# Optimization experiments

Hardware: AMD Instinct MI355X
Metric: run time of the kernel (lower is better)

The kernel has to match this reference:

```python
import jax, jax.numpy as jnp
import numpy as np

N, D, B = 500000, 128, 2048

def setup_inputs() -> dict:
    key = jax.random.key(0)
    ks = jax.random.split(key, 7)
    x = jax.random.normal(ks[0], (N, D), dtype=jnp.float32)
    batch = jnp.sort(jax.random.randint(ks[1], (N,), 0, B)).astype(jnp.int64)
    s = 1.0 / np.sqrt(D)
    Wm = jax.random.uniform(ks[2], (D, D), jnp.float32, -s, s)  # xavier-ish
    fc1_w = jax.random.uniform(ks[3], (D // 4, D), jnp.float32, -s, s)
    fc1_b = jnp.zeros((D // 4,), jnp.float32)
    fc2_w = jax.random.uniform(ks[4], (D, D // 4), jnp.float32, -1/np.sqrt(D//4), 1/np.sqrt(D//4))
    fc2_b = jnp.zeros((D,), jnp.float32)
    return {"x": x, "batch": batch, "size": B, "Wm": Wm,
            "fc1_w": fc1_w, "fc1_b": fc1_b, "fc2_w": fc2_w, "fc2_b": fc2_b}

def reference(x, batch, size, Wm, fc1_w, fc1_b, fc2_w, fc2_b):
    batch = batch.astype(jnp.int32)
    # fc: Linear -> ReLU -> Linear -> Tanh
    attention = jnp.tanh(jax.nn.relu(x @ fc1_w.T + fc1_b) @ fc2_w.T + fc2_b)
    x2 = attention * x + x  # [N, D]
    # scatter_mean over graphs
    sums = jax.ops.segment_sum(x2, batch, num_segments=size)  # [B, D]
    cnt = jax.ops.segment_sum(jnp.ones((x2.shape[0],), x2.dtype), batch, num_segments=size)
    mean = sums / jnp.maximum(cnt, 1.0)[:, None]
    transformed_global = jnp.tanh(mean @ Wm)  # [B, D]
    coefs = jax.nn.sigmoid(jnp.sum(x2 * transformed_global[batch], axis=1))  # [N]
    weighted = coefs[:, None] * x2
    return jax.ops.segment_sum(weighted, batch, num_segments=size)  # [B, D]
```

## Files before the change

### kernel.cpp

```cpp
#include <hip/hip_runtime.h>
#include <math.h>

#define D 128
#define BLOCKS_A 768
#define BLOCKS_C 1536
#define THREADS 256

typedef short s8v __attribute__((ext_vector_type(8)));
typedef float f4v __attribute__((ext_vector_type(4)));

__device__ __forceinline__ float fast_tanh(float z) {
    float e = __expf(2.f * z);
    return 1.f - 2.f / (e + 1.f);
}
__device__ __forceinline__ unsigned cvt_pk_bf16(float lo, float hi) {
    unsigned r;
    asm("v_cvt_pk_bf16_f32 %0, %1, %2" : "=v"(r) : "v"(lo), "v"(hi));
    return r;
}
__device__ __forceinline__ s8v pack8(float4 w0, float4 w1) {
    union { unsigned u[4]; s8v v; } r;
    r.u[0] = cvt_pk_bf16(w0.x, w0.y);
    r.u[1] = cvt_pk_bf16(w0.z, w0.w);
    r.u[2] = cvt_pk_bf16(w1.x, w1.y);
    r.u[3] = cvt_pk_bf16(w1.z, w1.w);
    return r.v;
}

#define RFLUSH(ACC_, SEG_, DST_)                                              \
    if ((SEG_) >= 0) {                                                        \
        _Pragma("unroll")                                                     \
        for (int t = 0; t < 8; ++t) {                                         \
            ACC_[t] += __shfl_xor(ACC_[t], 16);                               \
            ACC_[t] += __shfl_xor(ACC_[t], 32);                               \
        }                                                                     \
        _Pragma("unroll")                                                     \
        for (int t = 0; t < 8; ++t)                                           \
            if ((t >> 1) == quad)                                             \
                atomicAdd(&(DST_)[(size_t)(SEG_) * 128 + m15 + 16 * t], ACC_[t]); \
    }

#define EPI0(RG_)                                                             \
    {                                                                         \
        int r = R + quad * 4 + RG_;                                           \
        int seg = batch[r];                                                   \
        const float* xrow = x + (size_t)r * 128 + m15;                        \
        float yv[8];                                                          \
        _Pragma("unroll")                                                     \
        for (int t = 0; t < 8; ++t) {                                         \
            float z = af[t][RG_] + b2l[t];                                    \
            yv[t] = xrow[16 * t] * (1.f + fast_tanh(z));                      \
        }                                                                     \
        union { unsigned u[4]; uint4 q; } pk;                                 \
        pk.u[0] = cvt_pk_bf16(yv[0], yv[1]);                                  \
        pk.u[1] = cvt_pk_bf16(yv[2], yv[3]);                                  \
        pk.u[2] = cvt_pk_bf16(yv[4], yv[5]);                                  \
        pk.u[3] = cvt_pk_bf16(yv[6], yv[7]);                                  \
        ((uint4*)x2s)[(size_t)b * 256 + RG_ * 64 + lane] = pk.q;              \
        if (seg == segLo) {                                                   \
            _Pragma("unroll")                                                 \
            for (int t = 0; t < 8; ++t) tl[t] += yv[t];                       \
        } else if (seg == segHi) {                                            \
            _Pragma("unroll")                                                 \
            for (int t = 0; t < 8; ++t) th[t] += yv[t];                       \
        } else {                                                              \
            _Pragma("unroll")                                                 \
            for (int t = 0; t < 8; ++t)                                       \
                atomicAdd(&sums[(size_t)seg * 128 + m15 + 16 * t], yv[t]);    \
        }                                                                     \
    }

__global__ __launch_bounds__(THREADS, 3) void phaseA(
    const float* __restrict__ x, const int* __restrict__ batch,
    const float* __restrict__ fc1_w, const float* __restrict__ fc1_b,
    const float* __restrict__ fc2_w, const float* __restrict__ fc2_b,
    float* __restrict__ sums, unsigned short* __restrict__ x2s, int N)
{
    __shared__ s8v wB1[2][4][64];
    __shared__ s8v wB2[8][64];
    __shared__ float hbuf[4][16 * 36];

    const int lane = threadIdx.x & 63;
    const int wv = threadIdx.x >> 6;
    const int m15 = lane & 15;
    const int quad = lane >> 4;

    if (wv == 0) {
        #pragma unroll
        for (int t = 0; t < 2; ++t)
            #pragma unroll
            for (int kc = 0; kc < 4; ++kc) {
                const float* p = fc1_w + (16 * t + m15) * 128 + kc * 32 + quad * 8;
                wB1[t][kc][lane] = pack8(*(const float4*)p, *(const float4*)(p + 4));
            }
        #pragma unroll
        for (int t = 0; t < 8; ++t) {
            const float* p = fc2_w + (16 * t + m15) * 32 + quad * 8;
            wB2[t][lane] = pack8(*(const float4*)p, *(const float4*)(p + 4));
        }
    }
    float b1l[2], b2l[8];
    #pragma unroll
    for (int t = 0; t < 2; ++t) b1l[t] = fc1_b[m15 + 16 * t];
    #pragma unroll
    for (int t = 0; t < 8; ++t) b2l[t] = fc2_b[m15 + 16 * t];
    __syncthreads();

    const int total16 = N >> 4;
    const int nw = BLOCKS_A * 4;
    const int gw = blockIdx.x * 4 + wv;
    const int base = total16 / nw, rem = total16 % nw;
    const int b0 = gw * base + (gw < rem ? gw : rem);
    const int b1e = b0 + base + (gw < rem ? 1 : 0);

    float* hw = hbuf[wv];

    float accW[8];
    #pragma unroll
    for (int t = 0; t < 8; ++t) accW[t] = 0.f;
    int curW = -1;
    const f4v z4 = {0.f, 0.f, 0.f, 0.f};

    float4 F[8];
    if (b0 < b1e) {
        const float* xp = x + (size_t)(b0 << 4) * D + m15 * 128 + quad * 8;
        #pragma unroll
        for (int kc = 0; kc < 4; ++kc) {
            F[2 * kc]     = *(const float4*)(xp + kc * 32);
            F[2 * kc + 1] = *(const float4*)(xp + kc * 32 + 4);
        }
    }

    for (int b = b0; b < b1e; ++b) {
        const int R = b << 4;
        s8v ax[4];
        #pragma unroll
        for (int kc = 0; kc < 4; ++kc)
            ax[kc] = pack8(F[2 * kc], F[2 * kc + 1]);
        if (b + 1 < b1e) {
            const float* xp = x + (size_t)((b + 1) << 4) * D + m15 * 128 + quad * 8;
            #pragma unroll
            for (int kc = 0; kc < 4; ++kc) {
                F[2 * kc]     = *(const float4*)(xp + kc * 32);
                F[2 * kc + 1] = *(const float4*)(xp + kc * 32 + 4);
            }
        }
        f4v accH[2];
        accH[0] = z4; accH[1] = z4;
        #pragma unroll
        for (int kc = 0; kc < 4; ++kc) {
            accH[0] = __builtin_amdgcn_mfma_f32_16x16x32_bf16(ax[kc], wB1[0][kc][lane], accH[0], 0, 0, 0);
            accH[1] = __builtin_amdgcn_mfma_f32_16x16x32_bf16(ax[kc], wB1[1][kc][lane], accH[1], 0, 0, 0);
        }
        #pragma unroll
        for (int t = 0; t < 2; ++t)
            #pragma unroll
            for (int rg = 0; rg < 4; ++rg) {
                float hv = fmaxf(accH[t][rg] + b1l[t], 0.f);
                hw[(quad * 4 + rg) * 36 + m15 + 16 * t] = hv;
            }
        const f4v h0 = *(const f4v*)&hw[m15 * 36 + quad * 8];
        const f4v h1 = *(const f4v*)&hw[m15 * 36 + quad * 8 + 4];
        union { unsigned u[4]; s8v v; } ahu;
        ahu.u[0] = cvt_pk_bf16(h0[0], h0[1]);
        ahu.u[1] = cvt_pk_bf16(h0[2], h0[3]);
        ahu.u[2] = cvt_pk_bf16(h1[0], h1[1]);
        ahu.u[3] = cvt_pk_bf16(h1[2], h1[3]);
        s8v ah = ahu.v;
        f4v af[8];
        #pragma unroll
        for (int t = 0; t < 8; ++t)
            af[t] = __builtin_amdgcn_mfma_f32_16x16x32_bf16(ah, wB2[t][lane], z4, 0, 0, 0);

        const int segLo = batch[R];
        const int segHi = batch[R + 15];
        float tl[8], th[8];
        #pragma unroll
        for (int t = 0; t < 8; ++t) { tl[t] = 0.f; th[t] = 0.f; }

        EPI0(0) EPI0(1) EPI0(2) EPI0(3)

        if (segLo == curW) {
            #pragma unroll
            for (int t = 0; t < 8; ++t) accW[t] += tl[t];
        } else {
            RFLUSH(accW, curW, sums)
            curW = segLo;
            #pragma unroll
            for (int t = 0; t < 8; ++t) accW[t] = tl[t];
        }
        if (segHi != segLo) {
            RFLUSH(accW, curW, sums)
            curW = segHi;
            #pragma unroll
            for (int t = 0; t < 8; ++t) accW[t] = th[t];
        }
    }
    RFLUSH(accW, curW, sums)
}

__global__ __launch_bounds__(D, 8) void phaseB(
    const float* __restrict__ sums, const int* __restrict__ batch,
    const float* __restrict__ Wm, float* __restrict__ tg, int N)
{
    int b = blockIdx.x;
    int d = threadIdx.x;
    __shared__ float m[D];
    __shared__ int bnd[2];
    if (d < 2) {
        int target = b + d;
        int lo = 0, hi = N;
        while (lo < hi) {
            int mid = (lo + hi) >> 1;
            if (batch[mid] < target) lo = mid + 1; else hi = mid;
        }
        bnd[d] = lo;
    }
    __syncthreads();
    float inv = 1.f / fmaxf((float)(bnd[1] - bnd[0]), 1.f);
    m[d] = sums[(b << 7) + d] * inv;
    __syncthreads();
    float acc = 0.f;
    #pragma unroll 8
    for (int k = 0; k < D; ++k)
        acc = fmaf(m[k], Wm[(k << 7) + d], acc);
    tg[(b << 7) + d] = fast_tanh(acc);
}

__device__ __forceinline__ float bf_lo(unsigned w) {
    union { unsigned u; float f; } v; v.u = w << 16; return v.f;
}
__device__ __forceinline__ float bf_hi(unsigned w) {
    union { unsigned u; float f; } v; v.u = w & 0xffff0000u; return v.f;
}

__global__ __launch_bounds__(THREADS, 4) void phaseC(
    const unsigned short* __restrict__ x2s, const int* __restrict__ batch,
    const float* __restrict__ tg, float* __restrict__ out, int N)
{
    const int lane = threadIdx.x & 63;
    const int wv = threadIdx.x >> 6;
    const int m15 = lane & 15;
    const int quad = lane >> 4;

    const int total16 = N >> 4;
    const int nw = BLOCKS_C * 4;
    const int gw = blockIdx.x * 4 + wv;
    const int base = total16 / nw, rem = total16 % nw;
    const int b0 = gw * base + (gw < rem ? gw : rem);
    const int b1e = b0 + base + (gw < rem ? 1 : 0);

    float accW[8], tgv[8];
    #pragma unroll
    for (int t = 0; t < 8; ++t) { accW[t] = 0.f; tgv[t] = 0.f; }
    int curW = -1;
    int curT = -1;

    for (int b = b0; b < b1e; ++b) {
        const int R = b << 4;
        const uint4* p = (const uint4*)x2s + (size_t)b * 256 + lane;
        uint4 C0 = p[0], C1 = p[64], C2 = p[128], C3 = p[192];
        const int segLo = batch[R];
        const int segHi = batch[R + 15];
        float tl[8], th[8];
        #pragma unroll
        for (int t = 0; t < 8; ++t) { tl[t] = 0.f; th[t] = 0.f; }

        #pragma unroll
        for (int rg = 0; rg < 4; ++rg) {
            uint4 C = rg == 0 ? C0 : rg == 1 ? C1 : rg == 2 ? C2 : C3;
            int seg = batch[R + quad * 4 + rg];
            if (seg != curT) {
                curT = seg;
                #pragma unroll
                for (int t = 0; t < 8; ++t)
                    tgv[t] = tg[(size_t)seg * 128 + m15 + 16 * t];
            }
            float xv[8];
            xv[0] = bf_lo(C.x); xv[1] = bf_hi(C.x);
            xv[2] = bf_lo(C.y); xv[3] = bf_hi(C.y);
            xv[4] = bf_lo(C.z); xv[5] = bf_hi(C.z);
            xv[6] = bf_lo(C.w); xv[7] = bf_hi(C.w);
            float dot = 0.f;
            #pragma unroll
            for (int t = 0; t < 8; ++t) dot = fmaf(xv[t], tgv[t], dot);
            dot += __shfl_xor(dot, 1);
            dot += __shfl_xor(dot, 2);
            dot += __shfl_xor(dot, 4);
            dot += __shfl_xor(dot, 8);
            float coef = 1.f / (1.f + __expf(-dot));
            if (seg == segLo) {
                #pragma unroll
                for (int t = 0; t < 8; ++t) tl[t] = fmaf(coef, xv[t], tl[t]);
            } else if (seg == segHi) {
                #pragma unroll
                for (int t = 0; t < 8; ++t) th[t] = fmaf(coef, xv[t], th[t]);
            } else {
                #pragma unroll
                for (int t = 0; t < 8; ++t)
                    atomicAdd(&out[(size_t)seg * 128 + m15 + 16 * t], coef * xv[t]);
            }
        }

        if (segLo == curW) {
            #pragma unroll
            for (int t = 0; t < 8; ++t) accW[t] += tl[t];
        } else {
            RFLUSH(accW, curW, out)
            curW = segLo;
            #pragma unroll
            for (int t = 0; t < 8; ++t) accW[t] = tl[t];
        }
        if (segHi != segLo) {
            RFLUSH(accW, curW, out)
            curW = segHi;
            #pragma unroll
            for (int t = 0; t < 8; ++t) accW[t] = th[t];
        }
    }
    RFLUSH(accW, curW, out)
}

extern "C" void kernel_launch(void* const* d_in, const int* in_sizes, int n_in,
                              void* d_out, int out_size, void* d_ws, size_t ws_size,
                              hipStream_t stream) {
    const float* x     = (const float*)d_in[0];
    const int*   batch = (const int*)d_in[1];
    const float* Wm    = (const float*)d_in[3];
    const float* fc1_w = (const float*)d_in[4];
    const float* fc1_b = (const float*)d_in[5];
    const float* fc2_w = (const float*)d_in[6];
    const float* fc2_b = (const float*)d_in[7];
    float* out = (float*)d_out;

    int N = in_sizes[0] / D;
    int B = out_size / D;

    float* sums = (float*)d_ws;
    float* tg   = sums + (size_t)B * D;
    unsigned short* x2s = (unsigned short*)(tg + (size_t)B * D);

    hipMemsetAsync(d_ws, 0, (size_t)B * D * sizeof(float), stream);
    hipMemsetAsync(d_out, 0, (size_t)out_size * sizeof(float), stream);

    phaseA<<<BLOCKS_A, THREADS, 0, stream>>>(
        x, batch, fc1_w, fc1_b, fc2_w, fc2_b, sums, x2s, N);
    phaseB<<<B, D, 0, stream>>>(sums, batch, Wm, tg, N);
    phaseC<<<BLOCKS_C, THREADS, 0, stream>>>(x2s, batch, tg, out, N);
}
```

Baseline: 447.7 us.

## Fuse three phases into one persistent kernel with software grid barriers

Merges phaseA, phaseB and phaseC into a single persistent kernel of 704 blocks. Two atomic-counter grid barriers separate the segment-sum, the per-graph transform and the weighted pass, and the output zeroing moves inside the kernel, removing one memset and two kernel launches. Each wave reuses the same row range in phase C as in phase A, so its x2 data may still sit in cache. The risks are deadlock if not all 704 blocks are co-resident, the cost of spin-wait barriers, and phase C running with fewer blocks than before.

```diff
diff --git a/kernel.cpp b/kernel.cpp
--- a/kernel.cpp
+++ b/kernel.cpp
@@ -2,9 +2,9 @@
 #include <math.h>
 
 #define D 128
-#define BLOCKS_A 768
-#define BLOCKS_C 1536
+#define BLOCKS 704
 #define THREADS 256
+#define NW (BLOCKS * 4)
 
 typedef short s8v __attribute__((ext_vector_type(8)));
 typedef float f4v __attribute__((ext_vector_type(4)));
@@ -25,6 +25,27 @@
     r.u[2] = cvt_pk_bf16(w1.x, w1.y);
     r.u[3] = cvt_pk_bf16(w1.z, w1.w);
     return r.v;
+}
+__device__ __forceinline__ float bf_lo(unsigned w) {
+    union { unsigned u; float f; } v; v.u = w << 16; return v.f;
+}
+__device__ __forceinline__ float bf_hi(unsigned w) {
+    union { unsigned u; float f; } v; v.u = w & 0xffff0000u; return v.f;
+}
+
+__device__ __forceinline__ void gridBarrier(unsigned* c, unsigned nblk) {
+    __syncthreads();
+    if (threadIdx.x == 0) {
+        __threadfence();
+        __hip_atomic_fetch_add(c, 1u, __ATOMIC_ACQ_REL, __HIP_MEMORY_SCOPE_AGENT);
+        unsigned v;
+        do {
+            __builtin_amdgcn_s_sleep(2);
+            v = __hip_atomic_load(c, __ATOMIC_RELAXED, __HIP_MEMORY_SCOPE_AGENT);
+        } while (v < nblk);
+        (void)__hip_atomic_load(c, __ATOMIC_ACQUIRE, __HIP_MEMORY_SCOPE_AGENT);
+    }
+    __syncthreads();
 }
 
 #define RFLUSH(ACC_, SEG_, DST_)                                              \
@@ -70,11 +91,13 @@
         }                                                                     \
     }
 
-__global__ __launch_bounds__(THREADS, 3) void phaseA(
+__global__ __launch_bounds__(THREADS, 3) void fusedABC(
     const float* __restrict__ x, const int* __restrict__ batch,
     const float* __restrict__ fc1_w, const float* __restrict__ fc1_b,
     const float* __restrict__ fc2_w, const float* __restrict__ fc2_b,
-    float* __restrict__ sums, unsigned short* __restrict__ x2s, int N)
+    const float* __restrict__ Wm, float* __restrict__ sums,
+    float* __restrict__ tg, unsigned short* __restrict__ x2s,
+    unsigned* __restrict__ ctr, float* __restrict__ out, int N, int B)
 {
     __shared__ s8v wB1[2][4][64];
     __shared__ s8v wB2[8][64];
@@ -107,218 +130,198 @@
     __syncthreads();
 
     const int total16 = N >> 4;
-    const int nw = BLOCKS_A * 4;
     const int gw = blockIdx.x * 4 + wv;
-    const int base = total16 / nw, rem = total16 % nw;
+    const int base = total16 / NW, rem = total16 % NW;
     const int b0 = gw * base + (gw < rem ? gw : rem);
     const int b1e = b0 + base + (gw < rem ? 1 : 0);
 
     float* hw = hbuf[wv];
-
-    float accW[8];
-    #pragma unroll
-    for (int t = 0; t < 8; ++t) accW[t] = 0.f;
-    int curW = -1;
     const f4v z4 = {0.f, 0.f, 0.f, 0.f};
 
-    float4 F[8];
-    if (b0 < b1e) {
-        const float* xp = x + (size_t)(b0 << 4) * D + m15 * 128 + quad * 8;
+    {
+        float accW[8];
         #pragma unroll
-        for (int kc = 0; kc < 4; ++kc) {
-            F[2 * kc]     = *(const float4*)(xp + kc * 32);
-            F[2 * kc + 1] = *(const float4*)(xp + kc * 32 + 4);
-        }
-    }
-
-    for (int b = b0; b < b1e; ++b) {
-        const int R = b << 4;
-        s8v ax[4];
-        #pragma unroll
-        for (int kc = 0; kc < 4; ++kc)
-            ax[kc] = pack8(F[2 * kc], F[2 * kc + 1]);
-        if (b + 1 < b1e) {
-            const float* xp = x + (size_t)((b + 1) << 4) * D + m15 * 128 + quad * 8;
+        for (int t = 0; t < 8; ++t) accW[t] = 0.f;
+        int curW = -1;
+
+        float4 F[8];
+        if (b0 < b1e) {
+            const float* xp = x + (size_t)(b0 << 4) * D + m15 * 128 + quad * 8;
             #pragma unroll
             for (int kc = 0; kc < 4; ++kc) {
                 F[2 * kc]     = *(const float4*)(xp + kc * 32);
                 F[2 * kc + 1] = *(const float4*)(xp + kc * 32 + 4);
             }
         }
-        f4v accH[2];
-        accH[0] = z4; accH[1] = z4;
+
+        for (int b = b0; b < b1e; ++b) {
+            const int R = b << 4;
+            s8v ax[4];
+            #pragma unroll
+            for (int kc = 0; kc < 4; ++kc)
+                ax[kc] = pack8(F[2 * kc], F[2 * kc + 1]);
+            if (b + 1 < b1e) {
+                const float* xp = x + (size_t)((b + 1) << 4) * D + m15 * 128 + quad * 8;
+                #pragma unroll
+                for (int kc = 0; kc < 4; ++kc) {
+                    F[2 * kc]     = *(const float4*)(xp + kc * 32);
+                    F[2 * kc + 1] = *(const float4*)(xp + kc * 32 + 4);
+                }
+            }
+            f4v accH[2];
+            accH[0] = z4; accH[1] = z4;
+            #pragma unroll
+            for (int kc = 0; kc < 4; ++kc) {
+                accH[0] = __builtin_amdgcn_mfma_f32_16x16x32_bf16(ax[kc], wB1[0][kc][lane], accH[0], 0, 0, 0);
+                accH[1] = __builtin_amdgcn_mfma_f32_16x16x32_bf16(ax[kc], wB1[1][kc][lane], accH[1], 0, 0, 0);
+            }
+            #pragma unroll
+            for (int t = 0; t < 2; ++t)
+                #pragma unroll
+                for (int rg = 0; rg < 4; ++rg) {
+                    float hv = fmaxf(accH[t][rg] + b1l[t], 0.f);
+                    hw[(quad * 4 + rg) * 36 + m15 + 16 * t] = hv;
+                }
+            const f4v h0 = *(const f4v*)&hw[m15 * 36 + quad * 8];
+            const f4v h1 = *(const f4v*)&hw[m15 * 36 + quad * 8 + 4];
+            union { unsigned u[4]; s8v v; } ahu;
+            ahu.u[0] = cvt_pk_bf16(h0[0], h0[1]);
+            ahu.u[1] = cvt_pk_bf16(h0[2], h0[3]);
+            ahu.u[2] = cvt_pk_bf16(h1[0], h1[1]);
+            ahu.u[3] = cvt_pk_bf16(h1[2], h1[3]);
+            s8v ah = ahu.v;
+            f4v af[8];
+            #pragma unroll
+            for (int t = 0; t < 8; ++t)
+                af[t] = __builtin_amdgcn_mfma_f32_16x16x32_bf16(ah, wB2[t][lane], z4, 0, 0, 0);
+
+            const int segLo = batch[R];
+            const int segHi = batch[R + 15];
+            float tl[8], th[8];
+            #pragma unroll
+            for (int t = 0; t < 8; ++t) { tl[t] = 0.f; th[t] = 0.f; }
+
+            EPI0(0) EPI0(1) EPI0(2) EPI0(3)
+
+            if (segLo == curW) {
+                #pragma unroll
+                for (int t = 0; t < 8; ++t) accW[t] += tl[t];
+            } else {
+                RFLUSH(accW, curW, sums)
+                curW = segLo;
+                #pragma unroll
+                for (int t = 0; t < 8; ++t) accW[t] = tl[t];
+            }
+            if (segHi != segLo) {
+                RFLUSH(accW, curW, sums)
+                curW = segHi;
+                #pragma unroll
+                for (int t = 0; t < 8; ++t) accW[t] = th[t];
+            }
+        }
+        RFLUSH(accW, curW, sums)
+    }
+
+    {
+        const int tot = B * D;
+        for (int i = blockIdx.x * THREADS + threadIdx.x; i < tot; i += BLOCKS * THREADS)
+            out[i] = 0.f;
+    }
+
+    gridBarrier(&ctr[0], BLOCKS);
+
+    if (gw < B) {
+        const int s = gw;
+        int lo0 = 0, hi0 = N;
+        while (lo0 < hi0) { int mid = (lo0 + hi0) >> 1; if (batch[mid] < s) lo0 = mid + 1; else hi0 = mid; }
+        int lo1 = lo0, hi1 = N;
+        while (lo1 < hi1) { int mid = (lo1 + hi1) >> 1; if (batch[mid] < s + 1) lo1 = mid + 1; else hi1 = mid; }
+        float invc = 1.f / fmaxf((float)(lo1 - lo0), 1.f);
+        hw[lane]      = sums[(size_t)s * 128 + lane] * invc;
+        hw[lane + 64] = sums[(size_t)s * 128 + lane + 64] * invc;
+        float a0 = 0.f, a1 = 0.f;
+        #pragma unroll 8
+        for (int k = 0; k < D; ++k) {
+            float mk = hw[k];
+            a0 = fmaf(mk, Wm[(size_t)k * 128 + lane], a0);
+            a1 = fmaf(mk, Wm[(size_t)k * 128 + lane + 64], a1);
+        }
+        tg[(size_t)s * 128 + lane]      = fast_tanh(a0);
+        tg[(size_t)s * 128 + lane + 64] = fast_tanh(a1);
+    }
+
+    gridBarrier(&ctr[1], BLOCKS);
+
+    {
+        float accW[8], tgv[8];
         #pragma unroll
-        for (int kc = 0; kc < 4; ++kc) {
-            accH[0] = __builtin_amdgcn_mfma_f32_16x16x32_bf16(ax[kc], wB1[0][kc][lane], accH[0], 0, 0, 0);
-            accH[1] = __builtin_amdgcn_mfma_f32_16x16x32_bf16(ax[kc], wB1[1][kc][lane], accH[1], 0, 0, 0);
-        }
-        #pragma unroll
-        for (int t = 0; t < 2; ++t)
+        for (int t = 0; t < 8; ++t) { accW[t] = 0.f; tgv[t] = 0.f; }
+        int curW = -1, curT = -1;
+
+        for (int b = b0; b < b1e; ++b) {
+            const int R = b << 4;
+            const uint4* p = (const uint4*)x2s + (size_t)b * 256 + lane;
+            uint4 C0 = p[0], C1 = p[64], C2 = p[128], C3 = p[192];
+            const int segLo = batch[R];
+            const int segHi = batch[R + 15];
+            float tl[8], th[8];
+            #pragma unroll
+            for (int t = 0; t < 8; ++t) { tl[t] = 0.f; th[t] = 0.f; }
+
             #pragma unroll
             for (int rg = 0; rg < 4; ++rg) {
-                float hv = fmaxf(accH[t][rg] + b1l[t], 0.f);
-                hw[(quad * 4 + rg) * 36 + m15 + 16 * t] = hv;
-            }
-        const f4v h0 = *(const f4v*)&hw[m15 * 36 + quad * 8];
-        const f4v h1 = *(const f4v*)&hw[m15 * 36 + quad * 8 + 4];
-        union { unsigned u[4]; s8v v; } ahu;
-        ahu.u[0] = cvt_pk_bf16(h0[0], h0[1]);
-        ahu.u[1] = cvt_pk_bf16(h0[2], h0[3]);
-        ahu.u[2] = cvt_pk_bf16(h1[0], h1[1]);
-        ahu.u[3] = cvt_pk_bf16(h1[2], h1[3]);
-        s8v ah = ahu.v;
-        f4v af[8];
-        #pragma unroll
-        for (int t = 0; t < 8; ++t)
-            af[t] = __builtin_amdgcn_mfma_f32_16x16x32_bf16(ah, wB2[t][lane], z4, 0, 0, 0);
-
-        const int segLo = batch[R];
-        const int segHi = batch[R + 15];
-        float tl[8], th[8];
-        #pragma unroll
-        for (int t = 0; t < 8; ++t) { tl[t] = 0.f; th[t] = 0.f; }
-
-        EPI0(0) EPI0(1) EPI0(2) EPI0(3)
-
-        if (segLo == curW) {
-            #pragma unroll
-            for (int t = 0; t < 8; ++t) accW[t] += tl[t];
-        } else {
-            RFLUSH(accW, curW, sums)
-            curW = segLo;
-            #pragma unroll
-            for (int t = 0; t < 8; ++t) accW[t] = tl[t];
-        }
-        if (segHi != segLo) {
-            RFLUSH(accW, curW, sums)
-            curW = segHi;
-            #pragma unroll
-            for (int t = 0; t < 8; ++t) accW[t] = th[t];
-        }
-    }
-    RFLUSH(accW, curW, sums)
-}
-
-__global__ __launch_bounds__(D, 8) void phaseB(
-    const float* __restrict__ sums, const int* __restrict__ batch,
-    const float* __restrict__ Wm, float* __restrict__ tg, int N)
-{
-    int b = blockIdx.x;
-    int d = threadIdx.x;
-    __shared__ float m[D];
-    __shared__ int bnd[2];
-    if (d < 2) {
-        int target = b + d;
-        int lo = 0, hi = N;
-        while (lo < hi) {
-            int mid = (lo + hi) >> 1;
-            if (batch[mid] < target) lo = mid + 1; else hi = mid;
-        }
-        bnd[d] = lo;
-    }
-    __syncthreads();
-    float inv = 1.f / fmaxf((float)(bnd[1] - bnd[0]), 1.f);
-    m[d] = sums[(b << 7) + d] * inv;
-    __syncthreads();
-    float acc = 0.f;
-    #pragma unroll 8
-    for (int k = 0; k < D; ++k)
-        acc = fmaf(m[k], Wm[(k << 7) + d], acc);
-    tg[(b << 7) + d] = fast_tanh(acc);
-}
-
-__device__ __forceinline__ float bf_lo(unsigned w) {
-    union { unsigned u; float f; } v; v.u = w << 16; return v.f;
-}
-__device__ __forceinline__ float bf_hi(unsigned w) {
-    union { unsigned u; float f; } v; v.u = w & 0xffff0000u; return v.f;
-}
-
-__global__ __launch_bounds__(THREADS, 4) void phaseC(
-    const unsigned short* __restrict__ x2s, const int* __restrict__ batch,
-    const float* __restrict__ tg, float* __restrict__ out, int N)
-{
-    const int lane = threadIdx.x & 63;
-    const int wv = threadIdx.x >> 6;
-    const int m15 = lane & 15;
-    const int quad = lane >> 4;
-
-    const int total16 = N >> 4;
-    const int nw = BLOCKS_C * 4;
-    const int gw = blockIdx.x * 4 + wv;
-    const int base = total16 / nw, rem = total16 % nw;
-    const int b0 = gw * base + (gw < rem ? gw : rem);
-    const int b1e = b0 + base + (gw < rem ? 1 : 0);
-
-    float accW[8], tgv[8];
-    #pragma unroll
-    for (int t = 0; t < 8; ++t) { accW[t] = 0.f; tgv[t] = 0.f; }
-    int curW = -1;
-    int curT = -1;
-
-    for (int b = b0; b < b1e; ++b) {
-        const int R = b << 4;
-        const uint4* p = (const uint4*)x2s + (size_t)b * 256 + lane;
-        uint4 C0 = p[0], C1 = p[64], C2 = p[128], C3 = p[192];
-        const int segLo = batch[R];
-        const int segHi = batch[R + 15];
-        float tl[8], th[8];
-        #pragma unroll
-        for (int t = 0; t < 8; ++t) { tl[t] = 0.f; th[t] = 0.f; }
-
-        #pragma unroll
-        for (int rg = 0; rg < 4; ++rg) {
-            uint4 C = rg == 0 ? C0 : rg == 1 ? C1 : rg == 2 ? C2 : C3;
-            int seg = batch[R + quad * 4 + rg];
-            if (seg != curT) {
-                curT = seg;
-                #pragma unroll
-                for (int t = 0; t < 8; ++t)
-                    tgv[t] = tg[(size_t)seg * 128 + m15 + 16 * t];
-            }
-            float xv[8];
-            xv[0] = bf_lo(C.x); xv[1] = bf_hi(C.x);
-            xv[2] = bf_lo(C.y); xv[3] = bf_hi(C.y);
-            xv[4] = bf_lo(C.z); xv[5] = bf_hi(C.z);
-            xv[6] = bf_lo(C.w); xv[7] = bf_hi(C.w);
-            float dot = 0.f;
-            #pragma unroll
-            for (int t = 0; t < 8; ++t) dot = fmaf(xv[t], tgv[t], dot);
-            dot += __shfl_xor(dot, 1);
-            dot += __shfl_xor(dot, 2);
-            dot += __shfl_xor(dot, 4);
-            dot += __shfl_xor(dot, 8);
-            float coef = 1.f / (1.f + __expf(-dot));
-            if (seg == segLo) {
-                #pragma unroll
-                for (int t = 0; t < 8; ++t) tl[t] = fmaf(coef, xv[t], tl[t]);
-            } else if (seg == segHi) {
-                #pragma unroll
-                for (int t = 0; t < 8; ++t) th[t] = fmaf(coef, xv[t], th[t]);
+                uint4 C = rg == 0 ? C0 : rg == 1 ? C1 : rg == 2 ? C2 : C3;
+                int seg = batch[R + quad * 4 + rg];
+                if (seg != curT) {
+                    curT = seg;
+                    #pragma unroll
+                    for (int t = 0; t < 8; ++t)
+                        tgv[t] = tg[(size_t)seg * 128 + m15 + 16 * t];
+                }
+                float xv[8];
+                xv[0] = bf_lo(C.x); xv[1] = bf_hi(C.x);
+                xv[2] = bf_lo(C.y); xv[3] = bf_hi(C.y);
+                xv[4] = bf_lo(C.z); xv[5] = bf_hi(C.z);
+                xv[6] = bf_lo(C.w); xv[7] = bf_hi(C.w);
+                float dot = 0.f;
+                #pragma unroll
+                for (int t = 0; t < 8; ++t) dot = fmaf(xv[t], tgv[t], dot);
+                dot += __shfl_xor(dot, 1);
+                dot += __shfl_xor(dot, 2);
+                dot += __shfl_xor(dot, 4);
+                dot += __shfl_xor(dot, 8);
+                float coef = 1.f / (1.f + __expf(-dot));
+                if (seg == segLo) {
+                    #pragma unroll
+                    for (int t = 0; t < 8; ++t) tl[t] = fmaf(coef, xv[t], tl[t]);
+                } else if (seg == segHi) {
+                    #pragma unroll
+                    for (int t = 0; t < 8; ++t) th[t] = fmaf(coef, xv[t], th[t]);
+                } else {
+                    #pragma unroll
+                    for (int t = 0; t < 8; ++t)
+                        atomicAdd(&out[(size_t)seg * 128 + m15 + 16 * t], coef * xv[t]);
+                }
+            }
+
+            if (segLo == curW) {
+                #pragma unroll
+                for (int t = 0; t < 8; ++t) accW[t] += tl[t];
             } else {
-                #pragma unroll
-                for (int t = 0; t < 8; ++t)
-                    atomicAdd(&out[(size_t)seg * 128 + m15 + 16 * t], coef * xv[t]);
-            }
-        }
-
-        if (segLo == curW) {
-            #pragma unroll
-            for (int t = 0; t < 8; ++t) accW[t] += tl[t];
-        } else {
-            RFLUSH(accW, curW, out)
-            curW = segLo;
-            #pragma unroll
-            for (int t = 0; t < 8; ++t) accW[t] = tl[t];
-        }
-        if (segHi != segLo) {
-            RFLUSH(accW, curW, out)
-            curW = segHi;
-            #pragma unroll
-            for (int t = 0; t < 8; ++t) accW[t] = th[t];
-        }
-    }
-    RFLUSH(accW, curW, out)
+                RFLUSH(accW, curW, out)
+                curW = segLo;
+                #pragma unroll
+                for (int t = 0; t < 8; ++t) accW[t] = tl[t];
+            }
+            if (segHi != segLo) {
+                RFLUSH(accW, curW, out)
+                curW = segHi;
+                #pragma unroll
+                for (int t = 0; t < 8; ++t) accW[t] = th[t];
+            }
+        }
+        RFLUSH(accW, curW, out)
+    }
 }
 
 extern "C" void kernel_launch(void* const* d_in, const int* in_sizes, int n_in,
@@ -337,14 +340,13 @@
     int B = out_size / D;
 
     float* sums = (float*)d_ws;
-    float* tg   = sums + (size_t)B * D;
+    unsigned* ctr = (unsigned*)((char*)d_ws + (size_t)B * D * 4);
+    float* tg = (float*)((char*)ctr + 64);
     unsigned short* x2s = (unsigned short*)(tg + (size_t)B * D);
 
-    hipMemsetAsync(d_ws, 0, (size_t)B * D * sizeof(float), stream);
-    hipMemsetAsync(d_out, 0, (size_t)out_size * sizeof(float), stream);
-
-    phaseA<<<BLOCKS_A, THREADS, 0, stream>>>(
-        x, batch, fc1_w, fc1_b, fc2_w, fc2_b, sums, x2s, N);
-    phaseB<<<B, D, 0, stream>>>(sums, batch, Wm, tg, N);
-    phaseC<<<BLOCKS_C, THREADS, 0, stream>>>(x2s, batch, tg, out, N);
-}
+    hipMemsetAsync(d_ws, 0, (size_t)B * D * 4 + 64, stream);
+
+    fusedABC<<<BLOCKS, THREADS, 0, stream>>>(
+        x, batch, fc1_w, fc1_b, fc2_w, fc2_b, Wm,
+        sums, tg, x2s, ctr, out, N, B);
+}
```

Measured after the change: 629.3 us. 40.6% more time.
